# Kernel optimization log

Hardware: AMD Instinct MI355X
Metric: run time of the kernel (lower is better)

The kernel has to match this reference:

```python
import jax, jax.numpy as jnp
import numpy as np

BIOSYNTHETIC_FAMILIES = {'glutamate': ['E','Q','P','R','K'], 'aspartate': ['D','N','T','I','M','K'], 'serine': ['S','G','C'], 'pyruvate': ['A','V','L'], 'aromatic': ['F','Y','W'], 'histidine': ['H']}
CODON_TABLE = {'UUU':'F','UUC':'F','UUA':'L','UUG':'L','CUU':'L','CUC':'L','CUA':'L','CUG':'L','AUU':'I','AUC':'I','AUA':'I','AUG':'M','GUU':'V','GUC':'V','GUA':'V','GUG':'V','UCU':'S','UCC':'S','UCA':'S','UCG':'S','CCU':'P','CCC':'P','CCA':'P','CCG':'P','ACU':'T','ACC':'T','ACA':'T','ACG':'T','GCU':'A','GCC':'A','GCA':'A','GCG':'A','UAU':'Y','UAC':'Y','UAA':'*','UAG':'*','CAU':'H','CAC':'H','CAA':'Q','CAG':'Q','AAU':'N','AAC':'N','AAA':'K','AAG':'K','GAU':'D','GAC':'D','GAA':'E','GAG':'E','UGU':'C','UGC':'C','UGA':'*','UGG':'W','CGU':'R','CGC':'R','CGA':'R','CGG':'R','AGU':'S','AGC':'S','AGA':'R','AGG':'R','GGU':'G','GGC':'G','GGA':'G','GGG':'G'}

def _family_matrix():
    # Replicates module __init__: later families overwrite earlier (e.g. K -> aspartate).
    aa2fam = {}
    for fam, aas in BIOSYNTHETIC_FAMILIES.items():
        for aa in aas:
            aa2fam[aa] = fam
    fam_ids = {f: i for i, f in enumerate(BIOSYNTHETIC_FAMILIES)}
    codons = list(CODON_TABLE.keys())
    fid = np.array([fam_ids.get(aa2fam.get(CODON_TABLE[c], None), -1) for c in codons], dtype=np.int32)
    mat = ((fid[:, None] == fid[None, :]) & (fid[:, None] >= 0)).astype(np.float32)
    return jnp.asarray(mat)  # [64, 64]

FAMILY_MATRIX = _family_matrix()

def setup_inputs() -> dict:
    key = jax.random.key(0)
    k1, k2 = jax.random.split(key)
    codon_embeddings = jax.random.normal(k1, (16, 512, 32), dtype=jnp.float32)
    codon_indices = jax.random.randint(k2, (16, 512), 0, 64, dtype=jnp.int64)
    return {'codon_embeddings': codon_embeddings, 'codon_indices': codon_indices}

def reference(codon_embeddings, codon_indices):
    b, s, d = codon_embeddings.shape
    x = codon_embeddings.reshape(-1, d)                 # [n, d]
    sq = jnp.sum(x * x, axis=-1)
    sqd = sq[:, None] + sq[None, :] - 2.0 * (x @ x.T)   # [n, n]
    sqd = jnp.maximum(sqd, 0.0)
    dist = jnp.where(sqd > 0, jnp.sqrt(jnp.where(sqd > 0, sqd, 1.0)), 0.0)
    idx = codon_indices.reshape(-1).astype(jnp.int32)   # all < 64 by construction
    same_family = FAMILY_MATRIX[idx[:, None], idx[None, :]]  # [n, n]
    same_sum = (dist * same_family).sum() / (same_family.sum() + 1e-10)
    diff_mask = 1.0 - same_family
    diff_sum = (dist * diff_mask).sum() / (diff_mask.sum() + 1e-10)
    loss = same_sum - 0.5 * diff_sum + 1.0
    return jax.nn.relu(loss)
```

## Files before the change

kernel.cpp:

```cpp
#include <hip/hip_runtime.h>

#define NPTS 8192
#define DIM  32
#define TILE 128
#define TPB  256
#define NT   (NPTS / TILE)
#define NBLK (NT * (NT + 1) / 2)
#define ROWS 72

typedef __attribute__((ext_vector_type(8))) short short8;
typedef __attribute__((ext_vector_type(4))) float floatx4;

__device__ const int FID[64] = {
    4,4,3,3, 3,3,3,3, 1,1,1,1, 3,3,3,3,
    2,2,2,2, 0,0,0,0, 1,1,1,1, 3,3,3,3,
    4,4,-1,-1, 5,5,0,0, 1,1,1,1, 1,1,0,0,
    2,2,-1,4, 0,0,0,0, 2,2,0,0, 2,2,2,2
};

__device__ __forceinline__ unsigned short bf16_rne(float f) {
    unsigned u = __float_as_uint(f);
    unsigned r = u + 0x7FFFu + ((u >> 16) & 1u);
    return (unsigned short)(r >> 16);
}
__device__ __forceinline__ float bf16_f(unsigned short h) {
    return __uint_as_float(((unsigned)h) << 16);
}

__global__ void prep_kernel(const float* __restrict__ x, const int* __restrict__ idx,
                            float* __restrict__ sq, int* __restrict__ fid) {
    int gid = blockIdx.x * blockDim.x + threadIdx.x;
    const float4* p = (const float4*)(x + (size_t)gid * DIM);
    float s = 0.f;
#pragma unroll
    for (int v = 0; v < 8; ++v) {
        float4 f = p[v];
        s += f.x * f.x + f.y * f.y + f.z * f.z + f.w * f.w;
    }
    sq[gid] = s;
    int f = FID[idx[gid] & 63];
    fid[gid] = (f >= 0) ? f : (-10 - gid);
}

__global__ __launch_bounds__(TPB, 2) void pair_kernel(const float* __restrict__ x,
                                                      const float* __restrict__ sq,
                                                      const int* __restrict__ fid,
                                                      double* __restrict__ partials) {
    __shared__ __align__(16) short Ash[TILE][ROWS];
    __shared__ __align__(16) short Bsh[TILE][ROWS];
    __shared__ double red[4][2];

    int b = blockIdx.x;
    int I = (int)((2 * NT + 1 - sqrtf((float)((2 * NT + 1) * (2 * NT + 1) - 8 * b))) * 0.5f);
    if (I < 0) I = 0;
    if (I > NT - 1) I = NT - 1;
    while ((I + 1) * NT - (I + 1) * I / 2 <= b) ++I;
    while (I * NT - I * (I - 1) / 2 > b) --I;
    int J = I + (b - (I * NT - I * (I - 1) / 2));
    int I0 = I * TILE, J0 = J * TILE;

    int tid = threadIdx.x;
    {
        int pnt = tid >> 1, h = tid & 1;
        const floatx4* srcA = (const floatx4*)(x + (size_t)(I0 + pnt) * DIM + h * 16);
        const floatx4* srcB = (const floatx4*)(x + (size_t)(J0 + pnt) * DIM + h * 16);
        float f[16];
#pragma unroll
        for (int side = 0; side < 2; ++side) {
            const floatx4* src = side ? srcB : srcA;
            short* dst = side ? &Bsh[pnt][0] : &Ash[pnt][0];
            *(floatx4*)&f[0]  = src[0];
            *(floatx4*)&f[4]  = src[1];
            *(floatx4*)&f[8]  = src[2];
            *(floatx4*)&f[12] = src[3];
            short8 hi0, hi1, lo0, lo1;
#pragma unroll
            for (int i = 0; i < 8; ++i) {
                unsigned short hb = bf16_rne(f[i]);
                unsigned short lb = bf16_rne(f[i] - bf16_f(hb));
                hi0[i] = (short)hb; lo0[i] = (short)lb;
            }
#pragma unroll
            for (int i = 0; i < 8; ++i) {
                unsigned short hb = bf16_rne(f[8 + i]);
                unsigned short lb = bf16_rne(f[8 + i] - bf16_f(hb));
                hi1[i] = (short)hb; lo1[i] = (short)lb;
            }
            *(short8*)&dst[h * 16]          = hi0;
            *(short8*)&dst[h * 16 + 8]      = hi1;
            *(short8*)&dst[32 + h * 16]     = lo0;
            *(short8*)&dst[32 + h * 16 + 8] = lo1;
        }
    }
    __syncthreads();

    int lane = tid & 63, w = tid >> 6;
    int r16 = lane & 15, kg = lane >> 4;

    short8 ah[2], al[2];
#pragma unroll
    for (int i = 0; i < 2; ++i) {
        int row = w * 32 + i * 16 + r16;
        ah[i] = *(const short8*)&Ash[row][kg * 8];
        al[i] = *(const short8*)&Ash[row][32 + kg * 8];
    }

    floatx4 acc[2][8];
#pragma unroll
    for (int i = 0; i < 2; ++i)
#pragma unroll
        for (int j = 0; j < 8; ++j) acc[i][j] = (floatx4)(0.f);

#pragma unroll
    for (int j = 0; j < 8; ++j) {
        int rowb = j * 16 + r16;
        short8 bh = *(const short8*)&Bsh[rowb][kg * 8];
        short8 bl = *(const short8*)&Bsh[rowb][32 + kg * 8];
#pragma unroll
        for (int i = 0; i < 2; ++i) {
            acc[i][j] = __builtin_amdgcn_mfma_f32_16x16x32_bf16(ah[i], bh, acc[i][j], 0, 0, 0);
            acc[i][j] = __builtin_amdgcn_mfma_f32_16x16x32_bf16(ah[i], bl, acc[i][j], 0, 0, 0);
            acc[i][j] = __builtin_amdgcn_mfma_f32_16x16x32_bf16(al[i], bh, acc[i][j], 0, 0, 0);
        }
    }

    float sqa[2][4]; int fa[2][4];
#pragma unroll
    for (int i = 0; i < 2; ++i)
#pragma unroll
        for (int r = 0; r < 4; ++r) {
            int row = I0 + w * 32 + i * 16 + kg * 4 + r;
            sqa[i][r] = sq[row]; fa[i][r] = fid[row];
        }
    float sqb[8]; int fb[8];
#pragma unroll
    for (int j = 0; j < 8; ++j) {
        int col = J0 + j * 16 + r16;
        sqb[j] = sq[col]; fb[j] = fid[col];
    }

    bool diagblk = (I == J);
    float s_all = 0.f, s_same = 0.f;
#pragma unroll
    for (int j = 0; j < 8; ++j) {
#pragma unroll
        for (int i = 0; i < 2; ++i) {
#pragma unroll
            for (int r = 0; r < 4; ++r) {
                float sqd = sqa[i][r] + sqb[j] - 2.f * acc[i][j][r];
                float dst = sqrtf(fmaxf(sqd, 0.f));
                if (diagblk) {
                    int lrow = w * 32 + i * 16 + kg * 4 + r;
                    int lcol = j * 16 + r16;
                    if (lrow >= lcol) dst = 0.f;
                }
                s_all += dst;
                s_same += (fa[i][r] == fb[j]) ? dst : 0.f;
            }
        }
    }
    s_all *= 2.f;
    s_same *= 2.f;

#pragma unroll
    for (int off = 32; off >= 1; off >>= 1) {
        s_all  += __shfl_xor(s_all, off);
        s_same += __shfl_xor(s_same, off);
    }
    if ((tid & 63) == 0) { red[w][0] = (double)s_all; red[w][1] = (double)s_same; }
    __syncthreads();
    if (tid == 0) {
        partials[2 * b]     = red[0][0] + red[1][0] + red[2][0] + red[3][0];
        partials[2 * b + 1] = red[0][1] + red[1][1] + red[2][1] + red[3][1];
    }
}

__global__ void reduce_kernel(const double* __restrict__ partials,
                              const int* __restrict__ idx,
                              float* __restrict__ out) {
    __shared__ double sh[4][2];
    __shared__ int hist[8];
    int tid = threadIdx.x;
    if (tid < 8) hist[tid] = 0;
    __syncthreads();
    for (int i = tid; i < NPTS; i += TPB) {
        int f = FID[idx[i] & 63];
        if (f >= 0) atomicAdd(&hist[f], 1);
    }

    double ta = 0.0, ts = 0.0;
    for (int i = tid; i < NBLK; i += TPB) {
        ta += partials[2 * i];
        ts += partials[2 * i + 1];
    }
#pragma unroll
    for (int off = 32; off >= 1; off >>= 1) {
        ta += __shfl_xor(ta, off);
        ts += __shfl_xor(ts, off);
    }
    if ((tid & 63) == 0) { sh[tid >> 6][0] = ta; sh[tid >> 6][1] = ts; }
    __syncthreads();
    if (tid == 0) {
        double s_all  = sh[0][0] + sh[1][0] + sh[2][0] + sh[3][0];
        double s_same = sh[0][1] + sh[1][1] + sh[2][1] + sh[3][1];
        double csame = 0.0;
#pragma unroll
        for (int f = 0; f < 6; ++f) csame += (double)hist[f] * (double)hist[f];
        double cdiff = (double)NPTS * (double)NPTS - csame;
        double same_mean = s_same / (csame + 1e-10);
        double diff_mean = (s_all - s_same) / (cdiff + 1e-10);
        double loss = same_mean - 0.5 * diff_mean + 1.0;
        out[0] = (float)(loss > 0.0 ? loss : 0.0);
    }
}

extern "C" void kernel_launch(void* const* d_in, const int* in_sizes, int n_in,
                              void* d_out, int out_size, void* d_ws, size_t ws_size,
                              hipStream_t stream) {
    const float* x  = (const float*)d_in[0];
    const int* idx  = (const int*)d_in[1];
    float* out      = (float*)d_out;

    double* partials = (double*)((char*)d_ws + 64);
    float* sq        = (float*)((char*)d_ws + 64 + NBLK * 2 * sizeof(double));
    int* fid         = (int*)((char*)d_ws + 64 + NBLK * 2 * sizeof(double) + NPTS * sizeof(float));

    prep_kernel<<<NPTS / TPB, TPB, 0, stream>>>(x, idx, sq, fid);
    pair_kernel<<<NBLK, TPB, 0, stream>>>(x, sq, fid, partials);
    reduce_kernel<<<1, TPB, 0, stream>>>(partials, idx, out);
}
```

Before: 49.23 us.

## Fuse squared-norm and family-id prep into pair kernel, drop prep launch

Removes the separate prep kernel. Each pair block now computes the squared norms of its two tiles from the fp32 values it already loads, and looks up their family ids, keeping both in shared memory. The epilogue reads these from LDS instead of global memory. This saves a kernel launch and the global round-trip for sq and fid, at the cost of some redundant per-block work. Launch bounds are also raised from 2 to 4 blocks per SIMD, which may force more register pressure.

```diff
diff --git a/kernel.cpp b/kernel.cpp
--- a/kernel.cpp
+++ b/kernel.cpp
@@ -27,27 +27,13 @@
     return __uint_as_float(((unsigned)h) << 16);
 }
 
-__global__ void prep_kernel(const float* __restrict__ x, const int* __restrict__ idx,
-                            float* __restrict__ sq, int* __restrict__ fid) {
-    int gid = blockIdx.x * blockDim.x + threadIdx.x;
-    const float4* p = (const float4*)(x + (size_t)gid * DIM);
-    float s = 0.f;
-#pragma unroll
-    for (int v = 0; v < 8; ++v) {
-        float4 f = p[v];
-        s += f.x * f.x + f.y * f.y + f.z * f.z + f.w * f.w;
-    }
-    sq[gid] = s;
-    int f = FID[idx[gid] & 63];
-    fid[gid] = (f >= 0) ? f : (-10 - gid);
-}
-
-__global__ __launch_bounds__(TPB, 2) void pair_kernel(const float* __restrict__ x,
-                                                      const float* __restrict__ sq,
-                                                      const int* __restrict__ fid,
+__global__ __launch_bounds__(TPB, 4) void pair_kernel(const float* __restrict__ x,
+                                                      const int* __restrict__ idx,
                                                       double* __restrict__ partials) {
     __shared__ __align__(16) short Ash[TILE][ROWS];
     __shared__ __align__(16) short Bsh[TILE][ROWS];
+    __shared__ float sqA[TILE], sqB[TILE];
+    __shared__ int   fA[TILE],  fB[TILE];
     __shared__ double red[4][2];
 
     int b = blockIdx.x;
@@ -65,6 +51,7 @@
         const floatx4* srcA = (const floatx4*)(x + (size_t)(I0 + pnt) * DIM + h * 16);
         const floatx4* srcB = (const floatx4*)(x + (size_t)(J0 + pnt) * DIM + h * 16);
         float f[16];
+        float sa = 0.f, sb = 0.f;
 #pragma unroll
         for (int side = 0; side < 2; ++side) {
             const floatx4* src = side ? srcB : srcA;
@@ -73,6 +60,10 @@
             *(floatx4*)&f[4]  = src[1];
             *(floatx4*)&f[8]  = src[2];
             *(floatx4*)&f[12] = src[3];
+            float s = 0.f;
+#pragma unroll
+            for (int i = 0; i < 16; ++i) s += f[i] * f[i];
+            if (side) sb = s; else sa = s;
             short8 hi0, hi1, lo0, lo1;
 #pragma unroll
             for (int i = 0; i < 8; ++i) {
@@ -91,6 +82,15 @@
             *(short8*)&dst[32 + h * 16]     = lo0;
             *(short8*)&dst[32 + h * 16 + 8] = lo1;
         }
+        sa += __shfl_xor(sa, 1);
+        sb += __shfl_xor(sb, 1);
+        if (h == 0) {
+            sqA[pnt] = sa; sqB[pnt] = sb;
+            int fa_ = FID[idx[I0 + pnt] & 63];
+            int fb_ = FID[idx[J0 + pnt] & 63];
+            fA[pnt] = (fa_ >= 0) ? fa_ : -(10 + I0 + pnt);
+            fB[pnt] = (fb_ >= 0) ? fb_ : -(10 + J0 + pnt);
+        }
     }
     __syncthreads();
 
@@ -129,14 +129,14 @@
     for (int i = 0; i < 2; ++i)
 #pragma unroll
         for (int r = 0; r < 4; ++r) {
-            int row = I0 + w * 32 + i * 16 + kg * 4 + r;
-            sqa[i][r] = sq[row]; fa[i][r] = fid[row];
+            int row = w * 32 + i * 16 + kg * 4 + r;
+            sqa[i][r] = sqA[row]; fa[i][r] = fA[row];
         }
     float sqb[8]; int fb[8];
 #pragma unroll
     for (int j = 0; j < 8; ++j) {
-        int col = J0 + j * 16 + r16;
-        sqb[j] = sq[col]; fb[j] = fid[col];
+        int col = j * 16 + r16;
+        sqb[j] = sqB[col]; fb[j] = fB[col];
     }
 
     bool diagblk = (I == J);
@@ -221,11 +221,8 @@
     const int* idx  = (const int*)d_in[1];
     float* out      = (float*)d_out;
 
-    double* partials = (double*)((char*)d_ws + 64);
-    float* sq        = (float*)((char*)d_ws + 64 + NBLK * 2 * sizeof(double));
-    int* fid         = (int*)((char*)d_ws + 64 + NBLK * 2 * sizeof(double) + NPTS * sizeof(float));
-
-    prep_kernel<<<NPTS / TPB, TPB, 0, stream>>>(x, idx, sq, fid);
-    pair_kernel<<<NBLK, TPB, 0, stream>>>(x, sq, fid, partials);
+    double* partials = (double*)d_ws;
+
+    pair_kernel<<<NBLK, TPB, 0, stream>>>(x, idx, partials);
     reduce_kernel<<<1, TPB, 0, stream>>>(partials, idx, out);
 }
```

New measurement: 45.59 us. -7.4%, faster.
